# Performance work log

Hardware: AMD Instinct MI355X
Metric: run time of the kernel (lower is better)

## Reference

```python
import jax, jax.numpy as jnp
import numpy as np

D = 768
H = 12
DH = 64
S = 1500
SCALE = 0.125  # 1/sqrt(64)


def setup_inputs() -> dict:
    key = jax.random.key(0)
    ks = jax.random.split(key, 8)
    def w(k):
        return jax.random.normal(k, (D, D), dtype=jnp.float32) * (1.0 / np.sqrt(D))
    x = jax.random.normal(ks[0], (8, S, D), dtype=jnp.float32)
    return {
        "x": x,
        "Wq": w(ks[1]), "bq": jax.random.normal(ks[2], (D,), dtype=jnp.float32) * 0.02,
        "Wk": w(ks[3]),
        "Wv": w(ks[4]), "bv": jax.random.normal(ks[5], (D,), dtype=jnp.float32) * 0.02,
        "Wo": w(ks[6]), "bo": jax.random.normal(ks[7], (D,), dtype=jnp.float32) * 0.02,
    }


def reference(x, Wq, bq, Wk, Wv, bv, Wo, bo):
    B = x.shape[0]
    # torch Linear: y = x @ W.T + b
    q = (jnp.einsum('bsd,ed->bse', x, Wq) + bq) * SCALE
    k = jnp.einsum('bsd,ed->bse', x, Wk)
    v = jnp.einsum('bsd,ed->bse', x, Wv) + bv
    # split heads: [B, S, H, DH] -> [B, H, S, DH]
    q = q.reshape(B, S, H, DH).transpose(0, 2, 1, 3)
    k = k.reshape(B, S, H, DH).transpose(0, 2, 1, 3)
    v = v.reshape(B, S, H, DH).transpose(0, 2, 1, 3)
    scores = jnp.einsum('bhqd,bhkd->bhqk', q, k)  # [B, H, S, S]
    probs = jax.nn.softmax(scores, axis=-1)
    ctx = jnp.einsum('bhqk,bhkd->bhqd', probs, v)
    ctx = ctx.transpose(0, 2, 1, 3).reshape(B, S, D)
    return jnp.einsum('bsd,ed->bse', ctx, Wo) + bo
```

## Files before the change

kernel.cpp:

```cpp
#include <hip/hip_runtime.h>
#include <hip/hip_bf16.h>

constexpr int kD  = 768;
constexpr int kH  = 12;
constexpr int kDH = 64;
constexpr int kS  = 1500;
constexpr int kSP = 1504;
constexpr int kB  = 8;
constexpr int kM  = kB * kS;
constexpr float kScale = 0.125f;
constexpr int kPSTR = 72;

typedef __bf16 bf16;
typedef __bf16 bf16x4 __attribute__((ext_vector_type(4)));
typedef __bf16 bf16x8 __attribute__((ext_vector_type(8)));
typedef float  floatx4 __attribute__((ext_vector_type(4)));

__global__ __launch_bounds__(256) void detect_kernel(const void* __restrict__ xraw,
                                                     int* __restrict__ flag) {
    __shared__ int bad;
    if (threadIdx.x == 0) bad = 0;
    __syncthreads();
    const bf16* xb = (const bf16*)xraw;
    int c = 0;
    for (int k = 0; k < 16; k++) {
        int idx = 2 * (threadIdx.x + 256 * k);
        float v = fabsf((float)xb[idx]);
        if (!(v == 0.0f || (v > 1e-20f && v < 1e6f))) c++;
    }
    atomicAdd(&bad, c);
    __syncthreads();
    if (threadIdx.x == 0) *flag = (bad > 8) ? 1 : 0;
}

__global__ __launch_bounds__(256) void cvt_bf16_kernel(const void* __restrict__ src,
                                                       bf16* __restrict__ dst, int n,
                                                       const int* __restrict__ flag) {
    int i = blockIdx.x * 256 + threadIdx.x;
    if (i < n) {
        if (*flag)
            dst[i] = (bf16)((const float*)src)[i];
        else
            dst[i] = ((const bf16*)src)[i];
    }
}

__global__ __launch_bounds__(256) void cvt_f32_kernel(const void* __restrict__ src,
                                                      float* __restrict__ dst, int n,
                                                      const int* __restrict__ flag) {
    int i = blockIdx.x * 256 + threadIdx.x;
    if (i < n) {
        if (*flag)
            dst[i] = ((const float*)src)[i];
        else
            dst[i] = (float)((const bf16*)src)[i];
    }
}

__global__ __launch_bounds__(256) void zeropad_kernel(bf16* __restrict__ q_ws,
                                                      bf16* __restrict__ k_ws,
                                                      bf16* __restrict__ vt_ws) {
    int t = blockIdx.x * 256 + threadIdx.x;
    if (t < kB * kH * (kSP - kS) * kDH) {
        int bh  = t >> 8;
        int rem = t & 255;
        int s   = kS + (rem >> 6);
        int dh  = rem & 63;
        size_t qi = ((size_t)bh * kSP + s) * kDH + dh;
        q_ws[qi] = (bf16)0.f;
        k_ws[qi] = (bf16)0.f;
        size_t vi = ((size_t)bh * kDH + dh) * kSP + s;
        vt_ws[vi] = (bf16)0.f;
    }
}

__device__ __forceinline__ void async_copy16(const bf16* g, bf16* l) {
    __builtin_amdgcn_global_load_lds(
        (const __attribute__((address_space(1))) void*)g,
        (__attribute__((address_space(3))) void*)l,
        16, 0, 0);
}

__device__ __forceinline__ void gemm128_core(const bf16* __restrict__ X,
                                             const bf16* __restrict__ W,
                                             int m0, int n0,
                                             bf16* Asm, bf16* Bsm,
                                             floatx4 acc[4][4]) {
    const int tid  = threadIdx.x;
    const int lane = tid & 63;
    const int w    = tid >> 6;
    const int srow = (w << 4) + (lane >> 2);
    const int scol = (lane & 3) << 3;
    const int lrow = lane & 15;
    const int lq   = lane >> 4;
    const int wm   = (w >> 1) << 6;
    const int wn   = (w & 1) << 6;

    const bf16* gA = X + (size_t)(m0 + srow) * kD + scol;
    const bf16* gB = W + (size_t)(n0 + srow) * kD + scol;
    bf16* lA = Asm + (w << 9);
    bf16* lB = Bsm + (w << 9);

    for (int k0 = 0; k0 < kD; k0 += 32) {
        async_copy16(gA + k0, lA);
        async_copy16(gA + (size_t)64 * kD + k0, lA + 2048);
        async_copy16(gB + k0, lB);
        async_copy16(gB + (size_t)64 * kD + k0, lB + 2048);
        __syncthreads();

        bf16x8 af[4], bfr[4];
#pragma unroll
        for (int i = 0; i < 4; i++)
            af[i] = *(const bf16x8*)(Asm + ((wm + i * 16 + lrow) << 5) + (lq << 3));
#pragma unroll
        for (int j = 0; j < 4; j++)
            bfr[j] = *(const bf16x8*)(Bsm + ((wn + j * 16 + lrow) << 5) + (lq << 3));
#pragma unroll
        for (int i = 0; i < 4; i++)
#pragma unroll
            for (int j = 0; j < 4; j++)
                acc[i][j] = __builtin_amdgcn_mfma_f32_16x16x32_bf16(
                    af[i], bfr[j], acc[i][j], 0, 0, 0);
        __syncthreads();
    }
}

__global__ __launch_bounds__(256) void qkv_kernel(const bf16* __restrict__ X,
                                                  const bf16* __restrict__ Wq,
                                                  const bf16* __restrict__ Wk,
                                                  const bf16* __restrict__ Wv,
                                                  const float* __restrict__ bq,
                                                  const float* __restrict__ bv,
                                                  bf16* __restrict__ q_ws,
                                                  bf16* __restrict__ k_ws,
                                                  bf16* __restrict__ vt_ws) {
    __shared__ bf16 Asm[128 * 32];
    __shared__ bf16 Bsm[128 * 32];

    const int m0  = blockIdx.x << 7;
    const int mat = blockIdx.y / 6;
    const int n0  = (blockIdx.y % 6) << 7;
    const bf16* W = (mat == 0) ? Wq : (mat == 1) ? Wk : Wv;

    floatx4 acc[4][4] = {};
    gemm128_core(X, W, m0, n0, Asm, Bsm, acc);

    const int tid  = threadIdx.x;
    const int lane = tid & 63;
    const int w    = tid >> 6;
    const int lrow = lane & 15;
    const int lq   = lane >> 4;
    const int wm   = (w >> 1) << 6;
    const int wn   = (w & 1) << 6;

#pragma unroll
    for (int i = 0; i < 4; i++) {
#pragma unroll
        for (int j = 0; j < 4; j++) {
            const int n  = n0 + wn + j * 16 + lrow;
            const int hh = n >> 6, dh = n & 63;
            const float bval = (mat == 0) ? bq[n] : (mat == 2) ? bv[n] : 0.f;
#pragma unroll
            for (int r = 0; r < 4; r++) {
                const int m = m0 + wm + i * 16 + lq * 4 + r;
                if (m >= kM) continue;
                float v = acc[i][j][r];
                if (mat == 0)      v = (v + bval) * kScale;
                else if (mat == 2) v = v + bval;
                const int bb = m / kS, s = m - bb * kS;
                if (mat == 2)
                    vt_ws[(((size_t)(bb * kH + hh)) * kDH + dh) * kSP + s] = (bf16)v;
                else if (mat == 1)
                    k_ws[(((size_t)(bb * kH + hh)) * kSP + s) * kDH + dh] = (bf16)v;
                else
                    q_ws[(((size_t)(bb * kH + hh)) * kSP + s) * kDH + dh] = (bf16)v;
            }
        }
    }
}

__global__ __launch_bounds__(256) void out_kernel(const bf16* __restrict__ X,
                                                  const bf16* __restrict__ Wo,
                                                  const float* __restrict__ bo,
                                                  float* __restrict__ outf) {
    __shared__ bf16 Asm[128 * 32];
    __shared__ bf16 Bsm[128 * 32];

    const int m0 = blockIdx.x << 7;
    const int n0 = blockIdx.y << 7;

    floatx4 acc[4][4] = {};
    gemm128_core(X, Wo, m0, n0, Asm, Bsm, acc);

    const int tid  = threadIdx.x;
    const int lane = tid & 63;
    const int w    = tid >> 6;
    const int lrow = lane & 15;
    const int lq   = lane >> 4;
    const int wm   = (w >> 1) << 6;
    const int wn   = (w & 1) << 6;

#pragma unroll
    for (int i = 0; i < 4; i++) {
#pragma unroll
        for (int j = 0; j < 4; j++) {
            const int n = n0 + wn + j * 16 + lrow;
            const float bval = bo[n];
#pragma unroll
            for (int r = 0; r < 4; r++) {
                const int m = m0 + wm + i * 16 + lq * 4 + r;
                if (m >= kM) continue;
                outf[(size_t)m * kD + n] = acc[i][j][r] + bval;
            }
        }
    }
}

__device__ __forceinline__ const bf16* lds_at(const bf16* sm, int row, int cb) {
    return sm + row * 64 + ((cb ^ ((row & 7) << 4)) >> 1);
}

__device__ __forceinline__ void stage_k(const bf16* __restrict__ kbase, int s0,
                                        bf16* ksm, int w, int lane) {
#pragma unroll
    for (int i = 0; i < 2; i++) {
        const int sidx = i * 4 + w;
        const int row  = sidx * 8 + (lane >> 3);
        const int cb   = (lane & 7) << 4;
        const int scb  = cb ^ ((row & 7) << 4);
        int gr = s0 + row;
        if (gr >= kSP) gr = 1472;
        async_copy16(kbase + (size_t)gr * kDH + (scb >> 1), ksm + sidx * 512);
    }
}

__device__ __forceinline__ void stage_v(const bf16* __restrict__ vbase, int s0,
                                        bf16* vsm, int w, int lane) {
#pragma unroll
    for (int i = 0; i < 2; i++) {
        const int sidx = i * 4 + w;
        const int row  = sidx * 8 + (lane >> 3);
        const int cb   = (lane & 7) << 4;
        const int scb  = cb ^ ((row & 7) << 4);
        int key = s0 + (scb >> 1);
        if (key >= kSP) key = 1472;
        async_copy16(vbase + (size_t)row * kSP + key, vsm + sidx * 512);
    }
}

__device__ __forceinline__ void qk_mfma_lds(const bf16* ksm,
                                            const bf16x8 qf[2][2],
                                            floatx4 sc[2][4],
                                            int col, int quad) {
#pragma unroll
    for (int t = 0; t < 4; t++) {
        const int r = 16 * t + col;
        const bf16x8 kf0 = *(const bf16x8*)lds_at(ksm, r, quad * 16);
        const bf16x8 kf1 = *(const bf16x8*)lds_at(ksm, r, 64 + quad * 16);
        __builtin_amdgcn_s_setprio(1);
#pragma unroll
        for (int qt = 0; qt < 2; qt++) {
            floatx4 a = {0.f, 0.f, 0.f, 0.f};
            a = __builtin_amdgcn_mfma_f32_16x16x32_bf16(kf0, qf[qt][0], a, 0, 0, 0);
            a = __builtin_amdgcn_mfma_f32_16x16x32_bf16(kf1, qf[qt][1], a, 0, 0, 0);
            sc[qt][t] = a;
        }
        __builtin_amdgcn_s_setprio(0);
    }
}

template <bool MASK>
__device__ __forceinline__ void exp_store(const floatx4 sc[2][4],
                                          bf16* __restrict__ Pw,
                                          float lsum[2],
                                          int s0, int col, int quad) {
#pragma unroll
    for (int qt = 0; qt < 2; qt++)
#pragma unroll
        for (int t = 0; t < 4; t++) {
            bf16x4 pv;
#pragma unroll
            for (int r = 0; r < 4; r++) {
                float p;
                if (MASK && (s0 + 16 * t + quad * 4 + r >= kS))
                    p = 0.f;
                else
                    p = __expf(sc[qt][t][r]);
                lsum[qt] += p;
                pv[r] = (bf16)p;
            }
            *(bf16x4*)(Pw + (qt * 16 + col) * kPSTR + 16 * t + quad * 4) = pv;
        }
}

__device__ __forceinline__ void pv_lds(const bf16* vsm,
                                       const bf16* __restrict__ Pr,
                                       floatx4 Oacc[2][4],
                                       int col, int quad) {
    bf16x8 pa[2][2];
#pragma unroll
    for (int qt = 0; qt < 2; qt++)
#pragma unroll
        for (int kc = 0; kc < 2; kc++)
            pa[qt][kc] = *(const bf16x8*)(Pr + (qt * 16 + col) * kPSTR + kc * 32 + quad * 8);
#pragma unroll
    for (int n = 0; n < 4; n++) {
        const int row = n * 16 + col;
#pragma unroll
        for (int kc = 0; kc < 2; kc++) {
            const bf16x8 vf = *(const bf16x8*)lds_at(vsm, row, kc * 64 + quad * 16);
            __builtin_amdgcn_s_setprio(1);
#pragma unroll
            for (int qt = 0; qt < 2; qt++)
                Oacc[qt][n] = __builtin_amdgcn_mfma_f32_16x16x32_bf16(
                    pa[qt][kc], vf, Oacc[qt][n], 0, 0, 0);
            __builtin_amdgcn_s_setprio(0);
        }
    }
}

__global__ __launch_bounds__(256, 2) void fattn_kernel(const bf16* __restrict__ q_ws,
                                                       const bf16* __restrict__ k_ws,
                                                       const bf16* __restrict__ vt_ws,
                                                       bf16* __restrict__ ctx) {
    __shared__ bf16 Ksm[2][64 * 64];
    __shared__ bf16 Vsm[2][64 * 64];
    __shared__ bf16 Pbuf[4][32 * kPSTR];

    const int idx = blockIdx.x;
    const int bh  = idx % 96;
    const int qb  = idx / 96;
    const int b   = bh / kH;
    const int h   = bh - b * kH;
    const int tid  = threadIdx.x;
    const int w    = tid >> 6;
    const int lane = tid & 63;
    const int col  = lane & 15;
    const int quad = lane >> 4;
    const int q0   = qb * 128 + w * 32;
    const bool active = (q0 < kS);

    const bf16* qbase = q_ws  + (size_t)bh * kSP * kDH;
    const bf16* kbase = k_ws  + (size_t)bh * kSP * kDH;
    const bf16* vbase = vt_ws + (size_t)bh * kDH * kSP;

    bf16x8 qf[2][2] = {};
    if (active) {
#pragma unroll
        for (int qt = 0; qt < 2; qt++) {
            const bf16* qr = qbase + (size_t)(q0 + qt * 16 + col) * kDH + quad * 8;
            qf[qt][0] = *(const bf16x8*)(qr);
            qf[qt][1] = *(const bf16x8*)(qr + 32);
        }
    }

    float lsum[2] = {0.f, 0.f};
    floatx4 Oacc[2][4];
#pragma unroll
    for (int qt = 0; qt < 2; qt++)
#pragma unroll
        for (int n = 0; n < 4; n++) Oacc[qt][n] = (floatx4){0.f, 0.f, 0.f, 0.f};

    bf16* const P = &Pbuf[w][0];
    floatx4 sc[2][4];

    stage_k(kbase, 0, &Ksm[0][0], w, lane);
    stage_v(vbase, 0, &Vsm[0][0], w, lane);
    __syncthreads();

    int buf = 0;
    for (int c = 0; c < 23; ++c) {
        stage_k(kbase, (c + 1) * 64, &Ksm[buf ^ 1][0], w, lane);
        stage_v(vbase, (c + 1) * 64, &Vsm[buf ^ 1][0], w, lane);
        if (active) {
            qk_mfma_lds(&Ksm[buf][0], qf, sc, col, quad);
            exp_store<false>(sc, P, lsum, c * 64, col, quad);
            pv_lds(&Vsm[buf][0], P, Oacc, col, quad);
        }
        __syncthreads();
        buf ^= 1;
    }
    if (active) {
        qk_mfma_lds(&Ksm[buf][0], qf, sc, col, quad);
        exp_store<true>(sc, P, lsum, 1472, col, quad);
        pv_lds(&Vsm[buf][0], P, Oacc, col, quad);

#pragma unroll
        for (int qt = 0; qt < 2; qt++) {
            float l = lsum[qt];
            l += __shfl_xor(l, 16);
            l += __shfl_xor(l, 32);
            const float rinv_col = 1.0f / l;
            float ri[4];
#pragma unroll
            for (int r = 0; r < 4; r++)
                ri[r] = __shfl(rinv_col, quad * 4 + r, 16);
#pragma unroll
            for (int n = 0; n < 4; n++)
#pragma unroll
                for (int r = 0; r < 4; r++) {
                    const int q = q0 + qt * 16 + quad * 4 + r;
                    if (q < kS)
                        ctx[((size_t)(b * kS + q)) * kD + h * kDH + n * 16 + col] =
                            (bf16)(Oacc[qt][n][r] * ri[r]);
                }
        }
    }
}

extern "C" void kernel_launch(void* const* d_in, const int* in_sizes, int n_in,
                              void* d_out, int out_size, void* d_ws, size_t ws_size,
                              hipStream_t stream) {
    float* out_f = (float*)d_out;

    constexpr size_t nX = (size_t)kM * kD;
    constexpr size_t nW = (size_t)kD * kD;
    constexpr size_t per_qkv = (size_t)kB * kH * kSP * kDH;

    bf16* xb    = (bf16*)d_ws;
    bf16* Wqb   = xb + nX;
    bf16* Wkb   = Wqb + nW;
    bf16* Wvb   = Wkb + nW;
    bf16* Wob   = Wvb + nW;
    bf16* q_ws  = Wob + nW;
    bf16* k_ws  = q_ws + per_qkv;
    bf16* vt_ws = k_ws + per_qkv;
    float* bqf  = (float*)(vt_ws + per_qkv);
    float* bvf  = bqf + kD;
    float* bof  = bvf + kD;
    int*  flag  = (int*)(bof + kD);
    bf16* ctx   = xb;

    detect_kernel<<<1, 256, 0, stream>>>(d_in[0], flag);
    cvt_bf16_kernel<<<(int)((nX + 255) / 256), 256, 0, stream>>>(d_in[0], xb,  (int)nX, flag);
    cvt_bf16_kernel<<<(int)((nW + 255) / 256), 256, 0, stream>>>(d_in[1], Wqb, (int)nW, flag);
    cvt_bf16_kernel<<<(int)((nW + 255) / 256), 256, 0, stream>>>(d_in[3], Wkb, (int)nW, flag);
    cvt_bf16_kernel<<<(int)((nW + 255) / 256), 256, 0, stream>>>(d_in[4], Wvb, (int)nW, flag);
    cvt_bf16_kernel<<<(int)((nW + 255) / 256), 256, 0, stream>>>(d_in[6], Wob, (int)nW, flag);
    cvt_f32_kernel<<<3, 256, 0, stream>>>(d_in[2], bqf, kD, flag);
    cvt_f32_kernel<<<3, 256, 0, stream>>>(d_in[5], bvf, kD, flag);
    cvt_f32_kernel<<<3, 256, 0, stream>>>(d_in[7], bof, kD, flag);

    zeropad_kernel<<<96, 256, 0, stream>>>(q_ws, k_ws, vt_ws);
    dim3 qkvgrid((kM + 127) / 128, 18);
    qkv_kernel<<<qkvgrid, 256, 0, stream>>>(xb, Wqb, Wkb, Wvb, bqf, bvf,
                                            q_ws, k_ws, vt_ws);

    fattn_kernel<<<dim3(12 * 96), 256, 0, stream>>>(q_ws, k_ws, vt_ws, ctx);

    dim3 ogrid((kM + 127) / 128, kD / 128);
    out_kernel<<<ogrid, 256, 0, stream>>>(ctx, Wob, bof, out_f);
}
```

Baseline: 351.9 us.

## Double-buffer GEMM LDS loads and remap QKV blocks for XCD locality

The shared GEMM core now uses two LDS buffers, issuing the async global-to-LDS copies for the next K slice before computing on the current one. The aim is to overlap memory latency with MFMA work, at the cost of twice the LDS per block. The QKV kernel also moves to a 1D grid with a remapped block index ((lin&7)*212 + lin>>3). This likely groups tiles that share the same X rows onto the same XCD for L2 reuse. Blocks past the 94*18 real tiles exit early.

```diff
diff --git a/kernel.cpp b/kernel.cpp
--- a/kernel.cpp
+++ b/kernel.cpp
@@ -81,11 +81,11 @@
         16, 0, 0);
 }
 
-__device__ __forceinline__ void gemm128_core(const bf16* __restrict__ X,
-                                             const bf16* __restrict__ W,
-                                             int m0, int n0,
-                                             bf16* Asm, bf16* Bsm,
-                                             floatx4 acc[4][4]) {
+__device__ __forceinline__ void gemm128_db(const bf16* __restrict__ X,
+                                           const bf16* __restrict__ W,
+                                           int m0, int n0,
+                                           bf16* Asm, bf16* Bsm,
+                                           floatx4 acc[4][4]) {
     const int tid  = threadIdx.x;
     const int lane = tid & 63;
     const int w    = tid >> 6;
@@ -98,30 +98,42 @@
 
     const bf16* gA = X + (size_t)(m0 + srow) * kD + scol;
     const bf16* gB = W + (size_t)(n0 + srow) * kD + scol;
-    bf16* lA = Asm + (w << 9);
-    bf16* lB = Bsm + (w << 9);
-
-    for (int k0 = 0; k0 < kD; k0 += 32) {
-        async_copy16(gA + k0, lA);
-        async_copy16(gA + (size_t)64 * kD + k0, lA + 2048);
-        async_copy16(gB + k0, lB);
-        async_copy16(gB + (size_t)64 * kD + k0, lB + 2048);
-        __syncthreads();
-
+    const int wof = w << 9;
+
+    async_copy16(gA, Asm + wof);
+    async_copy16(gA + (size_t)64 * kD, Asm + wof + 2048);
+    async_copy16(gB, Bsm + wof);
+    async_copy16(gB + (size_t)64 * kD, Bsm + wof + 2048);
+    asm volatile("s_waitcnt vmcnt(0)" ::: "memory");
+    __builtin_amdgcn_s_barrier();
+
+    for (int ks = 0; ks < kD / 32; ks++) {
+        const int cur = ks & 1;
+        if (ks + 1 < kD / 32) {
+            const int nb = (cur ^ 1) << 12;
+            const int k0 = (ks + 1) * 32;
+            async_copy16(gA + k0, Asm + nb + wof);
+            async_copy16(gA + (size_t)64 * kD + k0, Asm + nb + wof + 2048);
+            async_copy16(gB + k0, Bsm + nb + wof);
+            async_copy16(gB + (size_t)64 * kD + k0, Bsm + nb + wof + 2048);
+        }
+        const bf16* A = Asm + (cur << 12);
+        const bf16* B = Bsm + (cur << 12);
         bf16x8 af[4], bfr[4];
 #pragma unroll
         for (int i = 0; i < 4; i++)
-            af[i] = *(const bf16x8*)(Asm + ((wm + i * 16 + lrow) << 5) + (lq << 3));
+            af[i] = *(const bf16x8*)(A + ((wm + i * 16 + lrow) << 5) + (lq << 3));
 #pragma unroll
         for (int j = 0; j < 4; j++)
-            bfr[j] = *(const bf16x8*)(Bsm + ((wn + j * 16 + lrow) << 5) + (lq << 3));
+            bfr[j] = *(const bf16x8*)(B + ((wn + j * 16 + lrow) << 5) + (lq << 3));
 #pragma unroll
         for (int i = 0; i < 4; i++)
 #pragma unroll
             for (int j = 0; j < 4; j++)
                 acc[i][j] = __builtin_amdgcn_mfma_f32_16x16x32_bf16(
                     af[i], bfr[j], acc[i][j], 0, 0, 0);
-        __syncthreads();
+        asm volatile("s_waitcnt vmcnt(0)" ::: "memory");
+        __builtin_amdgcn_s_barrier();
     }
 }
 
@@ -134,16 +146,21 @@
                                                   bf16* __restrict__ q_ws,
                                                   bf16* __restrict__ k_ws,
                                                   bf16* __restrict__ vt_ws) {
-    __shared__ bf16 Asm[128 * 32];
-    __shared__ bf16 Bsm[128 * 32];
-
-    const int m0  = blockIdx.x << 7;
-    const int mat = blockIdx.y / 6;
-    const int n0  = (blockIdx.y % 6) << 7;
+    __shared__ bf16 Asm[2 * 4096];
+    __shared__ bf16 Bsm[2 * 4096];
+
+    const int lin = blockIdx.x;
+    const int wk  = (lin & 7) * 212 + (lin >> 3);
+    if (wk >= 94 * 18) return;
+    const int bx  = wk / 18;
+    const int r   = wk - bx * 18;
+    const int m0  = bx << 7;
+    const int mat = r / 6;
+    const int n0  = (r % 6) << 7;
     const bf16* W = (mat == 0) ? Wq : (mat == 1) ? Wk : Wv;
 
     floatx4 acc[4][4] = {};
-    gemm128_core(X, W, m0, n0, Asm, Bsm, acc);
+    gemm128_db(X, W, m0, n0, Asm, Bsm, acc);
 
     const int tid  = threadIdx.x;
     const int lane = tid & 63;
@@ -161,10 +178,10 @@
             const int hh = n >> 6, dh = n & 63;
             const float bval = (mat == 0) ? bq[n] : (mat == 2) ? bv[n] : 0.f;
 #pragma unroll
-            for (int r = 0; r < 4; r++) {
-                const int m = m0 + wm + i * 16 + lq * 4 + r;
+            for (int r2 = 0; r2 < 4; r2++) {
+                const int m = m0 + wm + i * 16 + lq * 4 + r2;
                 if (m >= kM) continue;
-                float v = acc[i][j][r];
+                float v = acc[i][j][r2];
                 if (mat == 0)      v = (v + bval) * kScale;
                 else if (mat == 2) v = v + bval;
                 const int bb = m / kS, s = m - bb * kS;
@@ -183,14 +200,14 @@
                                                   const bf16* __restrict__ Wo,
                                                   const float* __restrict__ bo,
                                                   float* __restrict__ outf) {
-    __shared__ bf16 Asm[128 * 32];
-    __shared__ bf16 Bsm[128 * 32];
+    __shared__ bf16 Asm[2 * 4096];
+    __shared__ bf16 Bsm[2 * 4096];
 
     const int m0 = blockIdx.x << 7;
     const int n0 = blockIdx.y << 7;
 
     floatx4 acc[4][4] = {};
-    gemm128_core(X, Wo, m0, n0, Asm, Bsm, acc);
+    gemm128_db(X, Wo, m0, n0, Asm, Bsm, acc);
 
     const int tid  = threadIdx.x;
     const int lane = tid & 63;
@@ -442,9 +459,8 @@
     cvt_f32_kernel<<<3, 256, 0, stream>>>(d_in[7], bof, kD, flag);
 
     zeropad_kernel<<<96, 256, 0, stream>>>(q_ws, k_ws, vt_ws);
-    dim3 qkvgrid((kM + 127) / 128, 18);
-    qkv_kernel<<<qkvgrid, 256, 0, stream>>>(xb, Wqb, Wkb, Wvb, bqf, bvf,
-                                            q_ws, k_ws, vt_ws);
+    qkv_kernel<<<dim3(1696), 256, 0, stream>>>(xb, Wqb, Wkb, Wvb, bqf, bvf,
+                                               q_ws, k_ws, vt_ws);
 
     fattn_kernel<<<dim3(12 * 96), 256, 0, stream>>>(q_ws, k_ws, vt_ws, ctx);
 
```

After: 356.3 us. No clear change (+1.3%).
